# Performance work log

Measured on AMD Instinct MI355X. Metric: run time of the kernel, lower is better.

Reference implementation:

```python
import jax, jax.numpy as jnp
import numpy as np

B, T, F, U4 = 4096, 72, 64, 1024  # U4 = 4*units, units=256


def setup_inputs() -> dict:
    key = jax.random.key(0)
    ks = jax.random.split(key, 5)
    return {
        "inputs": jax.random.normal(ks[0], (B, T, F), jnp.float32),
        "W": jax.random.normal(ks[1], (F, U4), jnp.float32) * 0.05,   # input kernel [F, 4U]
        "U": jax.random.normal(ks[2], (U4 // 4, U4), jnp.float32) * 0.05,  # recurrent kernel [U, 4U]
        "b": jnp.zeros((U4,), jnp.float32),
        "Wd": jax.random.normal(ks[3], (U4 // 4, F), jnp.float32) * 0.05,  # dense [U, F]
        "bd": jnp.zeros((F,), jnp.float32),
        "out_steps": 24,
    }


def _lstm_step(h, c, x, W, U, b):
    # Keras LSTMCell gate order: i, f, g(candidate), o
    z = x @ W + h @ U + b  # [B, 4U]
    i, f, g, o = jnp.split(z, 4, axis=-1)
    i = jax.nn.sigmoid(i)
    f = jax.nn.sigmoid(f)
    o = jax.nn.sigmoid(o)
    c_new = f * c + i * jnp.tanh(g)
    h_new = o * jnp.tanh(c_new)
    return h_new, c_new


def reference(inputs, W, U, b, Wd, bd, out_steps):
    units = U.shape[0]
    Bt = inputs.shape[0]
    h0 = jnp.zeros((Bt, units), inputs.dtype)
    c0 = jnp.zeros((Bt, units), inputs.dtype)

    # ---- warmup: run RNN over the input sequence ----
    def warm_body(carry, x_t):
        h, c = carry
        h, c = _lstm_step(h, c, x_t, W, U, b)
        return (h, c), None

    (h, c), _ = jax.lax.scan(warm_body, (h0, c0), jnp.swapaxes(inputs, 0, 1))
    pred0 = h @ Wd + bd  # [B, F]

    def dec_body(carry, _):
        pred, h, c = carry
        h, c = _lstm_step(h, c, pred, W, U, b)
        pred = h @ Wd + bd
        return (pred, h, c), pred

    _, preds_rest = jax.lax.scan(dec_body, (pred0, h, c), None, length=out_steps - 1)
    preds = jnp.concatenate([pred0[None], preds_rest], axis=0)  # [out_steps, B, F]
    return jnp.transpose(preds, (1, 0, 2))  # [B, out_steps, F]
```

## Files before the change

### kernel.cpp

```cpp
#include <hip/hip_runtime.h>
#include <math.h>

constexpr int SEQ_T = 72;
constexpr int FDIM  = 64;
constexpr int UNITS = 256;
constexpr int U4    = 1024;
constexpr int BATCH = 4096;
constexpr int NKC   = 10;


constexpr int A_SH    = NKC * 4 * 64 * 8;
constexpr int WL_SH   = 6 * 4 * 4 * 64 * 8;
constexpr int HST_SH  = 2 * 4 * 64 * 8;
constexpr int LDS_BYTES = (A_SH + WL_SH + HST_SH) * 2;

using bf16x8 = __attribute__((ext_vector_type(8))) short;
using f32x4  = __attribute__((ext_vector_type(4))) float;

__device__ __forceinline__ float sigmoid_fast(float x) {
    return 1.0f / (1.0f + __expf(-x));
}
__device__ __forceinline__ float tanh_fast(float x) {
    float ax = fabsf(x);
    float e  = __expf(2.0f * ax);
    float t  = 1.0f - 2.0f / (e + 1.0f);
    return copysignf(t, x);
}
__device__ __forceinline__ unsigned short f2bf(float f) {
    union { float f; unsigned u; } v; v.f = f;
    unsigned r = (v.u + 0x7FFFu + ((v.u >> 16) & 1u)) >> 16;
    return (unsigned short)r;
}
__device__ __forceinline__ bf16x8 pack8(float4 a, float4 b) {
    bf16x8 p;
    p[0] = (short)f2bf(a.x); p[1] = (short)f2bf(a.y);
    p[2] = (short)f2bf(a.z); p[3] = (short)f2bf(a.w);
    p[4] = (short)f2bf(b.x); p[5] = (short)f2bf(b.y);
    p[6] = (short)f2bf(b.z); p[7] = (short)f2bf(b.w);
    return p;
}

__global__ void prep_wblob(const float* __restrict__ W, const float* __restrict__ U,
                           unsigned short* __restrict__ Wblob) {
    int id = blockIdx.x * 256 + threadIdx.x;
    int l    = id & 63;
    int g    = (id >> 6) & 3;
    int ug   = (id >> 8) & 3;
    int rest = id >> 10;
    int kc   = rest % 10, ub = rest / 10;
    int col  = g * 256 + ub * 64 + ug * 16 + (l & 15);
    int kb   = kc * 32 + (l >> 4) * 8;
    bf16x8 v;
    #pragma unroll
    for (int e = 0; e < 8; ++e) {
        int k = kb + e;
        float f = (k < FDIM) ? W[(size_t)k * U4 + col] : U[(size_t)(k - FDIM) * U4 + col];
        v[e] = (short)f2bf(f);
    }
    *reinterpret_cast<bf16x8*>(Wblob + (size_t)id * 8) = v;
}

__global__ void prep_wdblob(const float* __restrict__ Wd, unsigned short* __restrict__ Wdblob) {
    int id = blockIdx.x * 256 + threadIdx.x;
    int l   = id & 63;
    int kcd = (id >> 6) & 7;
    int ft  = id >> 9;
    int f   = ft * 16 + (l & 15);
    int kb  = kcd * 32 + (l >> 4) * 8;
    bf16x8 v;
    #pragma unroll
    for (int e = 0; e < 8; ++e)
        v[e] = (short)f2bf(Wd[(size_t)(kb + e) * FDIM + f]);
    *reinterpret_cast<bf16x8*>(Wdblob + (size_t)id * 8) = v;
}

__device__ __forceinline__ unsigned long long agload(const unsigned long long* p) {
    return __hip_atomic_load(p, __ATOMIC_RELAXED, __HIP_MEMORY_SCOPE_AGENT);
}
__device__ __forceinline__ void agstore(unsigned long long* p, unsigned long long v) {
    __hip_atomic_store(p, v, __ATOMIC_RELAXED, __HIP_MEMORY_SCOPE_AGENT);
}

__global__ __launch_bounds__(512, 1) void lstm_persistent(
    const float* __restrict__ inputs,
    const float* __restrict__ bias,
    const unsigned short* __restrict__ Wblob,
    const unsigned short* __restrict__ Wdblob,
    const float* __restrict__ bd,
    unsigned short* __restrict__ hbuf,
    unsigned int* __restrict__ barcnt,
    float* __restrict__ out,
    int out_steps)
{
    extern __shared__ char smem[];
    unsigned short* A_s = (unsigned short*)smem;
    unsigned short* WL  = (unsigned short*)(smem + A_SH * 2);
    unsigned short* hst = (unsigned short*)(smem + (A_SH + WL_SH) * 2);

    const int tid  = threadIdx.x;
    const int w    = tid >> 6, lane = tid & 63;
    const int l16  = lane & 15, hi4 = lane >> 4;
    const int blk  = blockIdx.x;
    const int rg   = blk & 63, ub = blk >> 6;
    const int bb   = rg * 64;
    const int ug   = w & 3;
    const int m4a  = 2 * (w >> 2);

    {
        const unsigned short* src = Wblob + (size_t)(ub * 10) * 16 * 512;
        #pragma unroll
        for (int i = 0; i < 12; ++i) {
            int idx = (i * 512 + tid) * 8;
            *reinterpret_cast<bf16x8*>(WL + idx) =
                *reinterpret_cast<const bf16x8*>(src + idx);
        }
    }
    bf16x8 Breg[4][4];
    #pragma unroll
    for (int i = 0; i < 4; ++i)
        #pragma unroll
        for (int g = 0; g < 4; ++g)
            Breg[i][g] = *reinterpret_cast<const bf16x8*>(
                Wblob + ((size_t)(((ub * 10 + 6 + i) * 4 + ug) * 4 + g) * 64 + lane) * 8);

    const int uu = ub * 64 + ug * 16 + l16;
    float bz[4];
    #pragma unroll
    for (int g = 0; g < 4; ++g) bz[g] = bias[g * 256 + uu];
    const float bdv = bd[(w & 3) * 16 + l16];

    float c_reg[2][4];
    #pragma unroll
    for (int m = 0; m < 2; ++m)
        #pragma unroll
        for (int j = 0; j < 4; ++j) c_reg[m][j] = 0.0f;

    const int tmax = SEQ_T + out_steps - 1;
    const size_t HB = (size_t)64 * 16384;

    #pragma unroll 1
    for (int t = 0; ; ++t) {
        const int p = t & 1;

        if (t == 0) {
            #pragma unroll
            for (int i = 0; i < 8; ++i)
                *reinterpret_cast<unsigned long long*>(A_s + 4096 + (i * 512 + tid) * 4) = 0ull;
        } else {
            const unsigned long long* src = reinterpret_cast<const unsigned long long*>(
                hbuf + p * HB + (size_t)rg * 16384);
            unsigned long long vbuf[8];
            #pragma unroll
            for (int i = 0; i < 8; ++i) vbuf[i] = agload(src + (size_t)i * 512 + tid);
            #pragma unroll
            for (int i = 0; i < 8; ++i)
                *reinterpret_cast<unsigned long long*>(A_s + 4096 + (i * 512 + tid) * 4) = vbuf[i];
        }
        if (t < SEQ_T) {
            int r = tid >> 3, c8 = (tid & 7) * 8;
            const float* xr = inputs + ((size_t)(bb + r) * SEQ_T + t) * FDIM + c8;
            bf16x8 pk = pack8(*reinterpret_cast<const float4*>(xr),
                              *reinterpret_cast<const float4*>(xr + 4));
            int kcx = c8 >> 5;
            int lb  = (r & 15) | ((((c8 & 31) >> 3) & 3) << 4);
            *reinterpret_cast<bf16x8*>(A_s + ((kcx * 4 + (r >> 4)) * 64 + lb) * 8) = pk;
            __syncthreads();
        } else {
            __syncthreads();
            const int s = t - SEQ_T;
            const int f = (w & 3) * 16 + l16;
            f32x4 accp[2] = {{0.f,0.f,0.f,0.f},{0.f,0.f,0.f,0.f}};
            #pragma unroll
            for (int kcd = 0; kcd < 8; ++kcd) {
                bf16x8 bw = *reinterpret_cast<const bf16x8*>(
                    Wdblob + (size_t)((((w & 3) * 8 + kcd) * 64) + lane) * 8);
                #pragma unroll
                for (int m = 0; m < 2; ++m) {
                    bf16x8 a = *reinterpret_cast<const bf16x8*>(
                        A_s + (((2 + kcd) * 4 + (m4a + m)) * 64 + lane) * 8);
                    accp[m] = __builtin_amdgcn_mfma_f32_16x16x32_bf16(a, bw, accp[m], 0, 0, 0);
                }
            }
            const int kcx = f >> 5;
            const int lsh = (((f & 31) >> 3) & 3) << 4;
            #pragma unroll
            for (int m = 0; m < 2; ++m) {
                #pragma unroll
                for (int j = 0; j < 4; ++j) {
                    int row = (m4a + m) * 16 + hi4 * 4 + j;
                    float v = accp[m][j] + bdv;
                    if (ub == 0)
                        out[((size_t)(bb + row) * out_steps + s) * FDIM + f] = v;
                    A_s[((kcx * 4 + (row >> 4)) * 64 + ((row & 15) | lsh)) * 8 + (f & 7)] = f2bf(v);
                }
            }
            if (t == tmax) break;
            __syncthreads();
        }

        f32x4 acc[2][4];
        #pragma unroll
        for (int m = 0; m < 2; ++m)
            #pragma unroll
            for (int g = 0; g < 4; ++g) acc[m][g] = (f32x4){0.f, 0.f, 0.f, 0.f};

        #pragma unroll
        for (int kc = 0; kc < NKC; ++kc) {
            bf16x8 a0 = *reinterpret_cast<const bf16x8*>(
                A_s + ((kc * 4 + m4a) * 64 + lane) * 8);
            bf16x8 a1 = *reinterpret_cast<const bf16x8*>(
                A_s + ((kc * 4 + m4a + 1) * 64 + lane) * 8);
            #pragma unroll
            for (int g = 0; g < 4; ++g) {
                bf16x8 bw = (kc < 6)
                    ? *reinterpret_cast<const bf16x8*>(
                          WL + (((kc * 4 + ug) * 4 + g) * 64 + lane) * 8)
                    : Breg[kc - 6][g];
                acc[0][g] = __builtin_amdgcn_mfma_f32_16x16x32_bf16(a0, bw, acc[0][g], 0, 0, 0);
                acc[1][g] = __builtin_amdgcn_mfma_f32_16x16x32_bf16(a1, bw, acc[1][g], 0, 0, 0);
            }
        }

        const int kcb = (w & 3) >> 1;
        const int lsh2 = ((((w & 3) & 1) * 2 + (l16 >> 3)) & 3) << 4;
        #pragma unroll
        for (int m = 0; m < 2; ++m) {
            #pragma unroll
            for (int j = 0; j < 4; ++j) {
                float zi = acc[m][0][j] + bz[0];
                float zf = acc[m][1][j] + bz[1];
                float zg = acc[m][2][j] + bz[2];
                float zo = acc[m][3][j] + bz[3];
                float ig = sigmoid_fast(zi);
                float fg = sigmoid_fast(zf);
                float og = sigmoid_fast(zo);
                float cn = fg * c_reg[m][j] + ig * tanh_fast(zg);
                c_reg[m][j] = cn;
                float hv = og * tanh_fast(cn);
                int rl = hi4 * 4 + j;
                hst[((kcb * 4 + (m4a + m)) * 64 + (rl | lsh2)) * 8 + (l16 & 7)] = f2bf(hv);
            }
        }
        __syncthreads();

        {
            unsigned long long* dst = reinterpret_cast<unsigned long long*>(
                hbuf + (1 - p) * HB + (size_t)rg * 16384 + (size_t)(2 * ub) * 2048);
            const unsigned long long* src = reinterpret_cast<const unsigned long long*>(hst);
            agstore(dst + tid,       src[tid]);
            agstore(dst + 512 + tid, src[512 + tid]);
        }

        __syncthreads();
        if (tid == 0) {
            unsigned int* cnt = barcnt + rg * 32;
            __hip_atomic_fetch_add(cnt, 1u, __ATOMIC_RELAXED, __HIP_MEMORY_SCOPE_AGENT);
            const unsigned target = 4u * (unsigned)(t + 1);
            while (__hip_atomic_load(cnt, __ATOMIC_RELAXED, __HIP_MEMORY_SCOPE_AGENT) < target)
                __builtin_amdgcn_s_sleep(2);
        }
        __syncthreads();
    }
}

extern "C" void kernel_launch(void* const* d_in, const int* in_sizes, int n_in,
                              void* d_out, int out_size, void* d_ws, size_t ws_size,
                              hipStream_t stream) {
    const float* inputs = (const float*)d_in[0];
    const float* W      = (const float*)d_in[1];
    const float* U      = (const float*)d_in[2];
    const float* b      = (const float*)d_in[3];
    const float* Wd     = (const float*)d_in[4];
    const float* bd     = (const float*)d_in[5];
    float* out = (float*)d_out;

    const int out_steps = out_size / (BATCH * FDIM);

    char* ws = (char*)d_ws;
    unsigned short* Wblob  = (unsigned short*)(ws);
    unsigned short* Wdblob = (unsigned short*)(ws + (1u << 20));
    unsigned short* hbuf   = (unsigned short*)(ws + (2u << 20));
    unsigned int*   barcnt = (unsigned int*)(ws + (6u << 20));

    prep_wblob<<<160, 256, 0, stream>>>(W, U, Wblob);
    prep_wdblob<<<8, 256, 0, stream>>>(Wd, Wdblob);
    hipMemsetAsync(barcnt, 0, 64 * 128, stream);

    (void)hipFuncSetAttribute((const void*)lstm_persistent,
                              hipFuncAttributeMaxDynamicSharedMemorySize, LDS_BYTES);

    lstm_persistent<<<dim3(256), dim3(512), LDS_BYTES, stream>>>(
        inputs, b, Wblob, Wdblob, bd, hbuf, barcnt, out, out_steps);
}
```

Measured before the change: 562.0 us.

## Use per-block flag barrier, prefetch inputs, and fold log2e into weights

Replaces the atomic-counter group barrier with per-block step flags: each block stores its step number and four threads poll the four sibling flags. The next timestep's input row is loaded into registers right after the barrier so the global load overlaps the recurrent matmul. Gate activations now use exp2 and hardware reciprocal, with log2(e) folded into the packed weights and bias, which removes a multiply per exponential. Scaling before bf16 rounding slightly changes the rounding of the weights.

```diff
diff --git a/kernel.cpp b/kernel.cpp
--- a/kernel.cpp
+++ b/kernel.cpp
@@ -7,6 +7,7 @@
 constexpr int U4    = 1024;
 constexpr int BATCH = 4096;
 constexpr int NKC   = 10;
+constexpr float LOG2E = 1.4426950408889634f;
 
 
 constexpr int A_SH    = NKC * 4 * 64 * 8;
@@ -16,14 +17,17 @@
 
 using bf16x8 = __attribute__((ext_vector_type(8))) short;
 using f32x4  = __attribute__((ext_vector_type(4))) float;
-
-__device__ __forceinline__ float sigmoid_fast(float x) {
-    return 1.0f / (1.0f + __expf(-x));
-}
-__device__ __forceinline__ float tanh_fast(float x) {
-    float ax = fabsf(x);
-    float e  = __expf(2.0f * ax);
-    float t  = 1.0f - 2.0f / (e + 1.0f);
+using ull    = unsigned long long;
+
+__device__ __forceinline__ float sig2(float x) {
+    return __builtin_amdgcn_rcpf(1.0f + exp2f(-x));
+}
+__device__ __forceinline__ float tanh2(float x) {
+    float t = 1.0f - 2.0f * __builtin_amdgcn_rcpf(exp2f(2.0f * fabsf(x)) + 1.0f);
+    return copysignf(t, x);
+}
+__device__ __forceinline__ float tanhc(float x) {
+    float t = 1.0f - 2.0f * __builtin_amdgcn_rcpf(exp2f(2.0f * LOG2E * fabsf(x)) + 1.0f);
     return copysignf(t, x);
 }
 __device__ __forceinline__ unsigned short f2bf(float f) {
@@ -55,7 +59,7 @@
     for (int e = 0; e < 8; ++e) {
         int k = kb + e;
         float f = (k < FDIM) ? W[(size_t)k * U4 + col] : U[(size_t)(k - FDIM) * U4 + col];
-        v[e] = (short)f2bf(f);
+        v[e] = (short)f2bf(f * LOG2E);
     }
     *reinterpret_cast<bf16x8*>(Wblob + (size_t)id * 8) = v;
 }
@@ -74,10 +78,10 @@
     *reinterpret_cast<bf16x8*>(Wdblob + (size_t)id * 8) = v;
 }
 
-__device__ __forceinline__ unsigned long long agload(const unsigned long long* p) {
+__device__ __forceinline__ ull agload(const ull* p) {
     return __hip_atomic_load(p, __ATOMIC_RELAXED, __HIP_MEMORY_SCOPE_AGENT);
 }
-__device__ __forceinline__ void agstore(unsigned long long* p, unsigned long long v) {
+__device__ __forceinline__ void agstore(ull* p, ull v) {
     __hip_atomic_store(p, v, __ATOMIC_RELAXED, __HIP_MEMORY_SCOPE_AGENT);
 }
 
@@ -88,7 +92,7 @@
     const unsigned short* __restrict__ Wdblob,
     const float* __restrict__ bd,
     unsigned short* __restrict__ hbuf,
-    unsigned int* __restrict__ barcnt,
+    unsigned int* __restrict__ flags,
     float* __restrict__ out,
     int out_steps)
 {
@@ -126,7 +130,7 @@
     const int uu = ub * 64 + ug * 16 + l16;
     float bz[4];
     #pragma unroll
-    for (int g = 0; g < 4; ++g) bz[g] = bias[g * 256 + uu];
+    for (int g = 0; g < 4; ++g) bz[g] = bias[g * 256 + uu] * LOG2E;
     const float bdv = bd[(w & 3) * 16 + l16];
 
     float c_reg[2][4];
@@ -137,6 +141,15 @@
 
     const int tmax = SEQ_T + out_steps - 1;
     const size_t HB = (size_t)64 * 16384;
+    unsigned int* flagp = flags + rg * 32;
+
+    const int xr = tid >> 3, xc8 = (tid & 7) * 8;
+    float4 xq0, xq1;
+    {
+        const float* xs = inputs + ((size_t)(bb + xr) * SEQ_T + 0) * FDIM + xc8;
+        xq0 = *reinterpret_cast<const float4*>(xs);
+        xq1 = *reinterpret_cast<const float4*>(xs + 4);
+    }
 
     #pragma unroll 1
     for (int t = 0; ; ++t) {
@@ -145,26 +158,28 @@
         if (t == 0) {
             #pragma unroll
             for (int i = 0; i < 8; ++i)
-                *reinterpret_cast<unsigned long long*>(A_s + 4096 + (i * 512 + tid) * 4) = 0ull;
+                *reinterpret_cast<ull*>(A_s + 4096 + (i * 512 + tid) * 4) = 0ull;
         } else {
-            const unsigned long long* src = reinterpret_cast<const unsigned long long*>(
+            const ull* src = reinterpret_cast<const ull*>(
                 hbuf + p * HB + (size_t)rg * 16384);
-            unsigned long long vbuf[8];
+            ull vbuf[8];
             #pragma unroll
             for (int i = 0; i < 8; ++i) vbuf[i] = agload(src + (size_t)i * 512 + tid);
             #pragma unroll
             for (int i = 0; i < 8; ++i)
-                *reinterpret_cast<unsigned long long*>(A_s + 4096 + (i * 512 + tid) * 4) = vbuf[i];
+                *reinterpret_cast<ull*>(A_s + 4096 + (i * 512 + tid) * 4) = vbuf[i];
         }
         if (t < SEQ_T) {
-            int r = tid >> 3, c8 = (tid & 7) * 8;
-            const float* xr = inputs + ((size_t)(bb + r) * SEQ_T + t) * FDIM + c8;
-            bf16x8 pk = pack8(*reinterpret_cast<const float4*>(xr),
-                              *reinterpret_cast<const float4*>(xr + 4));
-            int kcx = c8 >> 5;
-            int lb  = (r & 15) | ((((c8 & 31) >> 3) & 3) << 4);
-            *reinterpret_cast<bf16x8*>(A_s + ((kcx * 4 + (r >> 4)) * 64 + lb) * 8) = pk;
+            bf16x8 pk = pack8(xq0, xq1);
+            int kcx = xc8 >> 5;
+            int lb  = (xr & 15) | ((((xc8 & 31) >> 3) & 3) << 4);
+            *reinterpret_cast<bf16x8*>(A_s + ((kcx * 4 + (xr >> 4)) * 64 + lb) * 8) = pk;
             __syncthreads();
+            if (t + 1 < SEQ_T) {
+                const float* xs = inputs + ((size_t)(bb + xr) * SEQ_T + (t + 1)) * FDIM + xc8;
+                xq0 = *reinterpret_cast<const float4*>(xs);
+                xq1 = *reinterpret_cast<const float4*>(xs + 4);
+            }
         } else {
             __syncthreads();
             const int s = t - SEQ_T;
@@ -231,12 +246,12 @@
                 float zf = acc[m][1][j] + bz[1];
                 float zg = acc[m][2][j] + bz[2];
                 float zo = acc[m][3][j] + bz[3];
-                float ig = sigmoid_fast(zi);
-                float fg = sigmoid_fast(zf);
-                float og = sigmoid_fast(zo);
-                float cn = fg * c_reg[m][j] + ig * tanh_fast(zg);
+                float ig = sig2(zi);
+                float fg = sig2(zf);
+                float og = sig2(zo);
+                float cn = fg * c_reg[m][j] + ig * tanh2(zg);
                 c_reg[m][j] = cn;
-                float hv = og * tanh_fast(cn);
+                float hv = og * tanhc(cn);
                 int rl = hi4 * 4 + j;
                 hst[((kcb * 4 + (m4a + m)) * 64 + (rl | lsh2)) * 8 + (l16 & 7)] = f2bf(hv);
             }
@@ -244,20 +259,21 @@
         __syncthreads();
 
         {
-            unsigned long long* dst = reinterpret_cast<unsigned long long*>(
+            ull* dst = reinterpret_cast<ull*>(
                 hbuf + (1 - p) * HB + (size_t)rg * 16384 + (size_t)(2 * ub) * 2048);
-            const unsigned long long* src = reinterpret_cast<const unsigned long long*>(hst);
+            const ull* src = reinterpret_cast<const ull*>(hst);
             agstore(dst + tid,       src[tid]);
             agstore(dst + 512 + tid, src[512 + tid]);
         }
 
         __syncthreads();
-        if (tid == 0) {
-            unsigned int* cnt = barcnt + rg * 32;
-            __hip_atomic_fetch_add(cnt, 1u, __ATOMIC_RELAXED, __HIP_MEMORY_SCOPE_AGENT);
-            const unsigned target = 4u * (unsigned)(t + 1);
-            while (__hip_atomic_load(cnt, __ATOMIC_RELAXED, __HIP_MEMORY_SCOPE_AGENT) < target)
-                __builtin_amdgcn_s_sleep(2);
+        if (tid == 0)
+            __hip_atomic_store(flagp + ub, (unsigned)(t + 1),
+                               __ATOMIC_RELAXED, __HIP_MEMORY_SCOPE_AGENT);
+        if (tid < 4) {
+            while (__hip_atomic_load(flagp + tid, __ATOMIC_RELAXED,
+                                     __HIP_MEMORY_SCOPE_AGENT) < (unsigned)(t + 1))
+                __builtin_amdgcn_s_sleep(1);
         }
         __syncthreads();
     }
@@ -280,15 +296,15 @@
     unsigned short* Wblob  = (unsigned short*)(ws);
     unsigned short* Wdblob = (unsigned short*)(ws + (1u << 20));
     unsigned short* hbuf   = (unsigned short*)(ws + (2u << 20));
-    unsigned int*   barcnt = (unsigned int*)(ws + (6u << 20));
+    unsigned int*   flags  = (unsigned int*)(ws + (6u << 20));
 
     prep_wblob<<<160, 256, 0, stream>>>(W, U, Wblob);
     prep_wdblob<<<8, 256, 0, stream>>>(Wd, Wdblob);
-    hipMemsetAsync(barcnt, 0, 64 * 128, stream);
+    hipMemsetAsync(flags, 0, 64 * 128, stream);
 
     (void)hipFuncSetAttribute((const void*)lstm_persistent,
                               hipFuncAttributeMaxDynamicSharedMemorySize, LDS_BYTES);
 
     lstm_persistent<<<dim3(256), dim3(512), LDS_BYTES, stream>>>(
-        inputs, b, Wblob, Wdblob, bd, hbuf, barcnt, out, out_steps);
-}
+        inputs, b, Wblob, Wdblob, bd, hbuf, flags, out, out_steps);
+}
```

Result: faster. 481.6 us (-14.3%).
